# Kernel tuning notes

Hardware: AMD Instinct MI355X
Metric: run time of the kernel (lower is better)

The kernel has to match this reference:

```python
import jax, jax.numpy as jnp
import numpy as np

B, S, D = 64, 2048, 512

def setup_inputs() -> dict:
    key = jax.random.key(0)
    k1, k2, k3, k4, k5 = jax.random.split(key, 5)
    x = jax.random.normal(k1, (B, S, D), dtype=jnp.float32)
    # torch Linear(dim, dim): weight [D, D], bias [D]
    W1 = jax.random.normal(k2, (D, D), dtype=jnp.float32) * (1.0 / np.sqrt(D))
    b1 = jax.random.normal(k3, (D,), dtype=jnp.float32) * 0.01
    # torch Linear(dim, 1): weight [1, D] -> stored as [D], bias scalar
    w2 = jax.random.normal(k4, (D,), dtype=jnp.float32) * (1.0 / np.sqrt(D))
    b2 = jax.random.normal(k5, (), dtype=jnp.float32) * 0.01
    return {"x": x, "W1": W1, "b1": b1, "w2": w2, "b2": b2}

def reference(x, W1, b1, w2, b2):
    # score MLP: Linear -> Tanh -> Linear(->1), squeeze
    h = jnp.tanh(jnp.einsum('bsd,ed->bse', x, W1) + b1)   # [B,S,D]
    scores = jnp.einsum('bsd,d->bs', h, w2) + b2          # [B,S]
    w = jax.nn.softmax(scores, axis=1)[..., None]         # [B,S,1]
    ctx = jnp.sum(x * w, axis=1)                          # [B,D]
    return (ctx, w)
```

## Files before the change

### kernel.cpp

```cpp
#include <hip/hip_runtime.h>
#include <hip/hip_bf16.h>

#define BB 64
#define SS 2048
#define DD 512
#define MTOT (BB * SS)

typedef __attribute__((ext_vector_type(8))) short short8;
typedef __attribute__((ext_vector_type(4))) float f32x4;

__device__ __forceinline__ short f2bf(float f){
  __hip_bfloat16 h = __float2bfloat16(f);
  return *reinterpret_cast<short*>(&h);
}
__device__ __forceinline__ short8 pack8(float4 a, float4 b){
  short8 u;
  u[0]=f2bf(a.x); u[1]=f2bf(a.y); u[2]=f2bf(a.z); u[3]=f2bf(a.w);
  u[4]=f2bf(b.x); u[5]=f2bf(b.y); u[6]=f2bf(b.z); u[7]=f2bf(b.w);
  return u;
}
__device__ __forceinline__ void gload_lds16(const unsigned short* g, unsigned short* l){
  __builtin_amdgcn_global_load_lds(
      (const __attribute__((address_space(1))) unsigned int*)g,
      (__attribute__((address_space(3))) unsigned int*)l, 16, 0, 0);
}

__global__ void cvt_w1_kernel(const float* __restrict__ W1, unsigned short* __restrict__ W1s){
  int i = blockIdx.x * blockDim.x + threadIdx.x;
  int s  = i >> 11;
  int g  = i & 2047;
  int kc = g >> 9;
  int e  = (g & 511) ^ kc;
  const float* src = W1 + (size_t)e * DD + s * 32 + kc * 8;
  float4 f0 = *(const float4*)src;
  float4 f1 = *(const float4*)(src + 4);
  *(short8*)(W1s + (size_t)i * 8) = pack8(f0, f1);
}

__launch_bounds__(512, 2)
__global__ void scores_kernel(const float* __restrict__ x,
                              const unsigned short* __restrict__ W1s,
                              const float* __restrict__ b1,
                              const float* __restrict__ w2,
                              float* __restrict__ scorep){
  __shared__ __align__(16) unsigned short Bbuf[2][16384];
  __shared__ __align__(16) unsigned short Abuf[2][4096];
  __shared__ float psum[8 * 128];

  const int t    = threadIdx.x;
  const int lane = t & 63;
  const int wid  = t >> 6;
  const int m0   = blockIdx.x * 128;
  const int arow = lane & 15;
  const int kgrp = lane >> 4;

  f32x4 acc[8][4];
  #pragma unroll
  for (int mt = 0; mt < 8; ++mt)
    #pragma unroll
    for (int et = 0; et < 4; ++et)
      acc[mt][et] = (f32x4){0.f, 0.f, 0.f, 0.f};

  const int ar = t >> 2;
  const int aq = t & 3;
  const float* asrc = x + (size_t)(m0 + ar) * DD + aq * 8;
  const int awoff = ((ar << 2) + (aq ^ ((ar >> 1) & 3))) << 4;

  const unsigned short* bsrc = W1s + ((size_t)((wid << 2) << 6) + lane) * 8;

  float4 areg[2][2];

  #pragma unroll
  for (int j = 0; j < 4; ++j)
    gload_lds16(bsrc + j * 512, &Bbuf[0][((wid << 2) + j) * 512]);
  float4 p0 = *(const float4*)asrc;
  float4 p1 = *(const float4*)(asrc + 4);
  areg[1][0] = *(const float4*)(asrc + 32);
  areg[1][1] = *(const float4*)(asrc + 36);
  *(short8*)((char*)&Abuf[0][0] + awoff) = pack8(p0, p1);
  asm volatile("s_waitcnt vmcnt(2)" ::: "memory");
  asm volatile("s_waitcnt lgkmcnt(0)" ::: "memory");
  __builtin_amdgcn_s_barrier();
  __builtin_amdgcn_sched_barrier(0);

  #pragma unroll
  for (int s = 0; s < 16; ++s){
    if (s < 15){
      const unsigned short* bs = bsrc + (size_t)(s + 1) * 16384;
      #pragma unroll
      for (int j = 0; j < 4; ++j)
        gload_lds16(bs + j * 512, &Bbuf[(s + 1) & 1][((wid << 2) + j) * 512]);
    }
    if (s < 14){
      areg[s & 1][0] = *(const float4*)(asrc + (s + 2) * 32);
      areg[s & 1][1] = *(const float4*)(asrc + (s + 2) * 32 + 4);
    }

    short8 bf[4];
    #pragma unroll
    for (int et = 0; et < 4; ++et){
      int e = (wid << 6) + (et << 4) + arow;
      bf[et] = *(const short8*)((char*)&Bbuf[s & 1][0] + (((kgrp << 9) + (e ^ kgrp)) << 4));
    }
    __builtin_amdgcn_s_setprio(1);
    #pragma unroll
    for (int mt = 0; mt < 8; ++mt){
      int row = mt * 16 + arow;
      short8 af = *(const short8*)((char*)&Abuf[s & 1][0]
                + (((row << 2) + (kgrp ^ ((row >> 1) & 3))) << 4));
      #pragma unroll
      for (int et = 0; et < 4; ++et)
        acc[mt][et] = __builtin_amdgcn_mfma_f32_16x16x32_bf16(af, bf[et], acc[mt][et], 0, 0, 0);
    }
    __builtin_amdgcn_s_setprio(0);

    if (s < 15)
      *(short8*)((char*)&Abuf[(s + 1) & 1][0] + awoff)
          = pack8(areg[(s + 1) & 1][0], areg[(s + 1) & 1][1]);

    if (s < 15){
      if (s < 14) asm volatile("s_waitcnt vmcnt(2)" ::: "memory");
      else        asm volatile("s_waitcnt vmcnt(0)" ::: "memory");
      asm volatile("s_waitcnt lgkmcnt(0)" ::: "memory");
      __builtin_amdgcn_s_barrier();
      __builtin_amdgcn_sched_barrier(0);
    }
  }

  float ps[8][4];
  #pragma unroll
  for (int mt = 0; mt < 8; ++mt)
    #pragma unroll
    for (int i = 0; i < 4; ++i) ps[mt][i] = 0.f;

  #pragma unroll
  for (int et = 0; et < 4; ++et){
    int e = (wid << 6) + (et << 4) + arow;
    float b1v = b1[e];
    float w2v = w2[e];
    #pragma unroll
    for (int mt = 0; mt < 8; ++mt){
      #pragma unroll
      for (int i = 0; i < 4; ++i){
        float g = acc[mt][et][i] + b1v;
        g = fminf(15.f, fmaxf(-15.f, g));
        float ex = __expf(2.f * g);
        ps[mt][i] += (1.f - 2.f / (ex + 1.f)) * w2v;
      }
    }
  }
  #pragma unroll
  for (int mt = 0; mt < 8; ++mt)
    #pragma unroll
    for (int i = 0; i < 4; ++i){
      float v = ps[mt][i];
      v += __shfl_xor(v, 1);
      v += __shfl_xor(v, 2);
      v += __shfl_xor(v, 4);
      v += __shfl_xor(v, 8);
      ps[mt][i] = v;
    }
  if ((lane & 15) == 0){
    #pragma unroll
    for (int mt = 0; mt < 8; ++mt)
      #pragma unroll
      for (int i = 0; i < 4; ++i)
        psum[wid * 128 + mt * 16 + (lane >> 4) * 4 + i] = ps[mt][i];
  }
  __syncthreads();
  if (t < 128){
    float ssum = 0.f;
    #pragma unroll
    for (int w = 0; w < 8; ++w) ssum += psum[w * 128 + t];
    scorep[m0 + t] = ssum;
  }
}

__global__ void softmax_kernel(const float* __restrict__ scorep, float* __restrict__ wout){
  const int b = blockIdx.x;
  const int t = threadIdx.x;
  float v[8];
  #pragma unroll
  for (int i = 0; i < 8; ++i) v[i] = scorep[(size_t)b * SS + t + i * 256];
  float m = v[0];
  #pragma unroll
  for (int i = 1; i < 8; ++i) m = fmaxf(m, v[i]);
  #pragma unroll
  for (int msk = 32; msk >= 1; msk >>= 1) m = fmaxf(m, __shfl_xor(m, msk));
  __shared__ float redm[4], reds[4];
  if ((t & 63) == 0) redm[t >> 6] = m;
  __syncthreads();
  m = fmaxf(fmaxf(redm[0], redm[1]), fmaxf(redm[2], redm[3]));
  float s = 0.f;
  #pragma unroll
  for (int i = 0; i < 8; ++i){ v[i] = __expf(v[i] - m); s += v[i]; }
  #pragma unroll
  for (int msk = 32; msk >= 1; msk >>= 1) s += __shfl_xor(s, msk);
  if ((t & 63) == 0) reds[t >> 6] = s;
  __syncthreads();
  s = reds[0] + reds[1] + reds[2] + reds[3];
  float inv = 1.f / s;
  #pragma unroll
  for (int i = 0; i < 8; ++i) wout[(size_t)b * SS + t + i * 256] = v[i] * inv;
}

__global__ void ctx_partial_kernel(const float* __restrict__ x, const float* __restrict__ wout,
                                   float* __restrict__ ctxp){
  __shared__ float red[4][512];
  const int t   = threadIdx.x;
  const int sub = t >> 7;
  const int dt  = t & 127;
  const int b   = blockIdx.x >> 3;
  const int sc  = blockIdx.x & 7;
  const float* xb = x + (size_t)b * SS * DD;
  const int s0 = sc * 256 + sub * 64;
  float4 acc = {0.f, 0.f, 0.f, 0.f};
  for (int s = s0; s < s0 + 64; ++s){
    float wv = wout[(size_t)b * SS + s];
    float4 xv = *(const float4*)(xb + (size_t)s * DD + dt * 4);
    acc.x += wv * xv.x; acc.y += wv * xv.y; acc.z += wv * xv.z; acc.w += wv * xv.w;
  }
  *(float4*)&red[sub][dt * 4] = acc;
  __syncthreads();
  if (t < 128){
    float4 r0 = *(const float4*)&red[0][t * 4];
    float4 r1 = *(const float4*)&red[1][t * 4];
    float4 r2 = *(const float4*)&red[2][t * 4];
    float4 r3 = *(const float4*)&red[3][t * 4];
    float4 o = { r0.x+r1.x+r2.x+r3.x, r0.y+r1.y+r2.y+r3.y,
                 r0.z+r1.z+r2.z+r3.z, r0.w+r1.w+r2.w+r3.w };
    *(float4*)&ctxp[((size_t)(b * 8 + sc)) * DD + t * 4] = o;
  }
}

__global__ void ctx_reduce_kernel(const float* __restrict__ ctxp, float* __restrict__ ctx){
  int i = blockIdx.x * blockDim.x + threadIdx.x;
  int b = i >> 9;
  int d = i & 511;
  float s = 0.f;
  #pragma unroll
  for (int sc = 0; sc < 8; ++sc) s += ctxp[((size_t)(b * 8 + sc)) * DD + d];
  ctx[(size_t)b * DD + d] = s;
}

extern "C" void kernel_launch(void* const* d_in, const int* in_sizes, int n_in,
                              void* d_out, int out_size, void* d_ws, size_t ws_size,
                              hipStream_t stream){
  const float* x  = (const float*)d_in[0];
  const float* W1 = (const float*)d_in[1];
  const float* b1 = (const float*)d_in[2];
  const float* w2 = (const float*)d_in[3];

  float* ctx  = (float*)d_out;
  float* wout = (float*)d_out + BB * DD;

  unsigned short* W1s = (unsigned short*)d_ws;
  float* scorep = (float*)((char*)d_ws + (512u << 10));
  float* ctxp   = (float*)d_ws;

  hipLaunchKernelGGL(cvt_w1_kernel,      dim3(128),  dim3(256), 0, stream, W1, W1s);
  hipLaunchKernelGGL(scores_kernel,      dim3(1024), dim3(512), 0, stream, x, W1s, b1, w2, scorep);
  hipLaunchKernelGGL(softmax_kernel,     dim3(64),   dim3(256), 0, stream, scorep, wout);
  hipLaunchKernelGGL(ctx_partial_kernel, dim3(512),  dim3(512), 0, stream, x, wout, ctxp);
  hipLaunchKernelGGL(ctx_reduce_kernel,  dim3(128),  dim3(256), 0, stream, ctxp, ctx);
}
```

Baseline: 181.5 us.

## Split scores GEMM output columns across two blocks to raise occupancy

Each scores block now computes half of the 512 hidden units (256 columns) for its 128 rows. The grid doubles to 2048 blocks, and the two partial score sums are written to separate buffers that the softmax kernel adds together. This halves the accumulator registers and the LDS B buffer so that 4 blocks can fit per CU instead of 2, aiming for better latency hiding. In exchange, each x tile is loaded and converted twice, and a second score buffer is written to and read from global memory.

```diff
diff --git a/kernel.cpp b/kernel.cpp
--- a/kernel.cpp
+++ b/kernel.cpp
@@ -27,38 +27,42 @@
 
 __global__ void cvt_w1_kernel(const float* __restrict__ W1, unsigned short* __restrict__ W1s){
   int i = blockIdx.x * blockDim.x + threadIdx.x;
-  int s  = i >> 11;
-  int g  = i & 2047;
-  int kc = g >> 9;
-  int e  = (g & 511) ^ kc;
+  int ec  = i >> 14;
+  int rem = i & 16383;
+  int s   = rem >> 10;
+  int g   = rem & 1023;
+  int kc  = g >> 8;
+  int el  = (g & 255) ^ kc;
+  int e   = (ec << 8) + el;
   const float* src = W1 + (size_t)e * DD + s * 32 + kc * 8;
   float4 f0 = *(const float4*)src;
   float4 f1 = *(const float4*)(src + 4);
   *(short8*)(W1s + (size_t)i * 8) = pack8(f0, f1);
 }
 
-__launch_bounds__(512, 2)
+__launch_bounds__(512, 4)
 __global__ void scores_kernel(const float* __restrict__ x,
                               const unsigned short* __restrict__ W1s,
                               const float* __restrict__ b1,
                               const float* __restrict__ w2,
                               float* __restrict__ scorep){
-  __shared__ __align__(16) unsigned short Bbuf[2][16384];
+  __shared__ __align__(16) unsigned short Bbuf[2][8192];
   __shared__ __align__(16) unsigned short Abuf[2][4096];
   __shared__ float psum[8 * 128];
 
   const int t    = threadIdx.x;
   const int lane = t & 63;
   const int wid  = t >> 6;
-  const int m0   = blockIdx.x * 128;
+  const int ec   = blockIdx.x & 1;
+  const int m0   = (blockIdx.x >> 1) * 128;
   const int arow = lane & 15;
   const int kgrp = lane >> 4;
 
-  f32x4 acc[8][4];
-  #pragma unroll
-  for (int mt = 0; mt < 8; ++mt)
-    #pragma unroll
-    for (int et = 0; et < 4; ++et)
+  f32x4 acc[8][2];
+  #pragma unroll
+  for (int mt = 0; mt < 8; ++mt)
+    #pragma unroll
+    for (int et = 0; et < 2; ++et)
       acc[mt][et] = (f32x4){0.f, 0.f, 0.f, 0.f};
 
   const int ar = t >> 2;
@@ -66,13 +70,13 @@
   const float* asrc = x + (size_t)(m0 + ar) * DD + aq * 8;
   const int awoff = ((ar << 2) + (aq ^ ((ar >> 1) & 3))) << 4;
 
-  const unsigned short* bsrc = W1s + ((size_t)((wid << 2) << 6) + lane) * 8;
+  const unsigned short* bsrc = W1s + ((size_t)ec * 131072) + ((size_t)(wid << 7) + lane) * 8;
 
   float4 areg[2][2];
 
   #pragma unroll
-  for (int j = 0; j < 4; ++j)
-    gload_lds16(bsrc + j * 512, &Bbuf[0][((wid << 2) + j) * 512]);
+  for (int j = 0; j < 2; ++j)
+    gload_lds16(bsrc + j * 512, &Bbuf[0][((wid << 1) + j) * 512]);
   float4 p0 = *(const float4*)asrc;
   float4 p1 = *(const float4*)(asrc + 4);
   areg[1][0] = *(const float4*)(asrc + 32);
@@ -86,21 +90,21 @@
   #pragma unroll
   for (int s = 0; s < 16; ++s){
     if (s < 15){
-      const unsigned short* bs = bsrc + (size_t)(s + 1) * 16384;
-      #pragma unroll
-      for (int j = 0; j < 4; ++j)
-        gload_lds16(bs + j * 512, &Bbuf[(s + 1) & 1][((wid << 2) + j) * 512]);
+      const unsigned short* bs = bsrc + (size_t)(s + 1) * 8192;
+      #pragma unroll
+      for (int j = 0; j < 2; ++j)
+        gload_lds16(bs + j * 512, &Bbuf[(s + 1) & 1][((wid << 1) + j) * 512]);
     }
     if (s < 14){
       areg[s & 1][0] = *(const float4*)(asrc + (s + 2) * 32);
       areg[s & 1][1] = *(const float4*)(asrc + (s + 2) * 32 + 4);
     }
 
-    short8 bf[4];
-    #pragma unroll
-    for (int et = 0; et < 4; ++et){
-      int e = (wid << 6) + (et << 4) + arow;
-      bf[et] = *(const short8*)((char*)&Bbuf[s & 1][0] + (((kgrp << 9) + (e ^ kgrp)) << 4));
+    short8 bf[2];
+    #pragma unroll
+    for (int et = 0; et < 2; ++et){
+      int el = (wid << 5) + (et << 4) + arow;
+      bf[et] = *(const short8*)((char*)&Bbuf[s & 1][0] + (((kgrp << 8) + (el ^ kgrp)) << 4));
     }
     __builtin_amdgcn_s_setprio(1);
     #pragma unroll
@@ -109,7 +113,7 @@
       short8 af = *(const short8*)((char*)&Abuf[s & 1][0]
                 + (((row << 2) + (kgrp ^ ((row >> 1) & 3))) << 4));
       #pragma unroll
-      for (int et = 0; et < 4; ++et)
+      for (int et = 0; et < 2; ++et)
         acc[mt][et] = __builtin_amdgcn_mfma_f32_16x16x32_bf16(af, bf[et], acc[mt][et], 0, 0, 0);
     }
     __builtin_amdgcn_s_setprio(0);
@@ -127,15 +131,20 @@
     }
   }
 
-  float ps[8][4];
-  #pragma unroll
-  for (int mt = 0; mt < 8; ++mt)
-    #pragma unroll
-    for (int i = 0; i < 4; ++i) ps[mt][i] = 0.f;
-
-  #pragma unroll
-  for (int et = 0; et < 4; ++et){
-    int e = (wid << 6) + (et << 4) + arow;
+  float ps[8][2];
+  #pragma unroll
+  for (int mt = 0; mt < 8; ++mt)
+    #pragma unroll
+    for (int i = 0; i < 2; ++i) ps[mt][i] = 0.f;
+  float psf[8][4];
+  #pragma unroll
+  for (int mt = 0; mt < 8; ++mt)
+    #pragma unroll
+    for (int i = 0; i < 4; ++i) psf[mt][i] = 0.f;
+
+  #pragma unroll
+  for (int et = 0; et < 2; ++et){
+    int e = (ec << 8) + (wid << 5) + (et << 4) + arow;
     float b1v = b1[e];
     float w2v = w2[e];
     #pragma unroll
@@ -145,7 +154,7 @@
         float g = acc[mt][et][i] + b1v;
         g = fminf(15.f, fmaxf(-15.f, g));
         float ex = __expf(2.f * g);
-        ps[mt][i] += (1.f - 2.f / (ex + 1.f)) * w2v;
+        psf[mt][i] += (1.f - 2.f / (ex + 1.f)) * w2v;
       }
     }
   }
@@ -153,26 +162,26 @@
   for (int mt = 0; mt < 8; ++mt)
     #pragma unroll
     for (int i = 0; i < 4; ++i){
-      float v = ps[mt][i];
+      float v = psf[mt][i];
       v += __shfl_xor(v, 1);
       v += __shfl_xor(v, 2);
       v += __shfl_xor(v, 4);
       v += __shfl_xor(v, 8);
-      ps[mt][i] = v;
+      psf[mt][i] = v;
     }
   if ((lane & 15) == 0){
     #pragma unroll
     for (int mt = 0; mt < 8; ++mt)
       #pragma unroll
       for (int i = 0; i < 4; ++i)
-        psum[wid * 128 + mt * 16 + (lane >> 4) * 4 + i] = ps[mt][i];
+        psum[wid * 128 + mt * 16 + (lane >> 4) * 4 + i] = psf[mt][i];
   }
   __syncthreads();
   if (t < 128){
     float ssum = 0.f;
     #pragma unroll
     for (int w = 0; w < 8; ++w) ssum += psum[w * 128 + t];
-    scorep[m0 + t] = ssum;
+    scorep[(size_t)ec * MTOT + m0 + t] = ssum;
   }
 }
 
@@ -181,7 +190,10 @@
   const int t = threadIdx.x;
   float v[8];
   #pragma unroll
-  for (int i = 0; i < 8; ++i) v[i] = scorep[(size_t)b * SS + t + i * 256];
+  for (int i = 0; i < 8; ++i){
+    int m = b * SS + t + i * 256;
+    v[i] = scorep[m] + scorep[MTOT + m];
+  }
   float m = v[0];
   #pragma unroll
   for (int i = 1; i < 8; ++i) m = fmaxf(m, v[i]);
@@ -259,7 +271,7 @@
   float* ctxp   = (float*)d_ws;
 
   hipLaunchKernelGGL(cvt_w1_kernel,      dim3(128),  dim3(256), 0, stream, W1, W1s);
-  hipLaunchKernelGGL(scores_kernel,      dim3(1024), dim3(512), 0, stream, x, W1s, b1, w2, scorep);
+  hipLaunchKernelGGL(scores_kernel,      dim3(2048), dim3(512), 0, stream, x, W1s, b1, w2, scorep);
   hipLaunchKernelGGL(softmax_kernel,     dim3(64),   dim3(256), 0, stream, scorep, wout);
   hipLaunchKernelGGL(ctx_partial_kernel, dim3(512),  dim3(512), 0, stream, x, wout, ctxp);
   hipLaunchKernelGGL(ctx_reduce_kernel,  dim3(128),  dim3(256), 0, stream, ctxp, ctx);
```

Measured after the change: 174.2 us. 4.0% less time.
